# Kernel optimization log

Measured on AMD Instinct MI355X. Metric: run time of the kernel, lower is better.

Reference implementation:

```python
import jax, jax.numpy as jnp
import numpy as np

# Norse default LIFParameters
TAU_SYN_INV = 200.0  # 1/5e-3
TAU_MEM_INV = 100.0  # 1/1e-2
V_LEAK = 0.0
V_TH = 1.0
V_RESET = 0.0
DT = 0.001


def _heaviside(x):
    return (x > 0).astype(x.dtype)


def setup_inputs() -> dict:
    key = jax.random.key(0)
    k1, k2 = jax.random.split(key)
    T, B, F = 1024, 256, 512
    input_spikes = (jax.random.uniform(k1, (T, B, F)) < 0.1).astype(jnp.float32)
    W = jax.random.normal(k2, (F, F), dtype=jnp.float32) / np.sqrt(F).astype(np.float32)
    return {"input_spikes": input_spikes, "W": W}


def reference(input_spikes, W):
    # input_spikes: [T, B, F]; W: [F, F] (Linear, no bias)
    T, B, F = input_spikes.shape
    # fc batched across the whole sequence (y = x @ W.T)
    xs = jnp.einsum('tbf,gf->tbg', input_spikes, W)  # [T, B, F]
    v0 = jnp.zeros((B, F), dtype=input_spikes.dtype)
    i0 = jnp.zeros((B, F), dtype=input_spikes.dtype)

    def step(carry, x):
        v, i = carry
        v_dec = v + DT * TAU_MEM_INV * ((V_LEAK - v) + i)  # membrane leak+integrate
        i_dec = i - DT * TAU_SYN_INV * i                   # synaptic current decay
        z = _heaviside(v_dec - V_TH)                       # spike
        v_new = (1.0 - z) * v_dec + z * V_RESET            # reset
        i_new = i_dec + x                                  # inject fc output
        return (v_new, i_new), z

    (v, i), zs = jax.lax.scan(step, (v0, i0), xs)
    # matches torch forward: returns (z_last, state) with state = (v, i)
    return zs[-1], v, i
```

## Files before the change

### kernel.cpp

```cpp
#include <hip/hip_runtime.h>
#include <hip/hip_bf16.h>


typedef __attribute__((ext_vector_type(8))) short short8;
typedef __attribute__((ext_vector_type(4))) float floatx4;
typedef __attribute__((ext_vector_type(2))) unsigned uintx2;
typedef __attribute__((ext_vector_type(4))) unsigned uintx4;

#define T_STEPS 1024
#define B_DIM   256
#define F_DIM   512
#define BF      (B_DIM * F_DIM)
#define ROWP    520

static __device__ __forceinline__ unsigned short f2bf_rne(float f) {
    unsigned u = __float_as_uint(f);
    return (unsigned short)((u + 0x7FFFu + ((u >> 16) & 1u)) >> 16);
}
static __device__ __forceinline__ float bf2f(unsigned short h) {
    return __uint_as_float(((unsigned)h) << 16);
}

__global__ __launch_bounds__(256)
void pack_kernel(const float* __restrict__ sp, unsigned* __restrict__ bits)
{
    const int lane = threadIdx.x & 63;
    const int wv   = blockIdx.x * 4 + (threadIdx.x >> 6);
    for (int c = wv; c < 65536; c += 2048 * 4) {
        const float* p = sp + (size_t)c * 2048;
        unsigned val = 0;
        #pragma unroll
        for (int r = 0; r < 32; ++r) {
            float x = p[r * 64 + lane];
            unsigned long long m = __ballot(x != 0.0f);
            unsigned sel = (lane & 1) ? (unsigned)(m >> 32) : (unsigned)m;
            if ((lane >> 1) == r) val = sel;
        }
        bits[(size_t)c * 64 + lane] = val;
    }
}

__global__ __launch_bounds__(512, 4)
void lif_kernel_bits(const unsigned* __restrict__ bits,
                     const float* __restrict__ W,
                     float* __restrict__ out)
{
    __shared__ float xbuf[2][7 * 256];

    const int tid  = threadIdx.x;
    const int lane = tid & 63;
    const int wq   = tid >> 6;
    const int bt   = blockIdx.x & 15;
    const int gb   = blockIdx.x >> 4;
    const int b0   = bt * 16;
    const int gw   = gb * 16;
    const int mrow = lane & 15;
    const int lq   = lane >> 4;
    const int bsh  = lq * 8;

    short8 whi[2], wmd[2], wlo[2];
    {
        const float* wp = W + (size_t)(gw + mrow) * F_DIM + wq * 64 + lq * 8;
        #pragma unroll
        for (int ks = 0; ks < 2; ++ks) {
            short8 hi, md, lo;
            #pragma unroll
            for (int j = 0; j < 8; ++j) {
                float f = wp[ks * 32 + j];
                unsigned short h = f2bf_rne(f);
                float r1 = f - bf2f(h);
                unsigned short m = f2bf_rne(r1);
                float r2 = r1 - bf2f(m);
                hi[j] = (short)h;
                md[j] = (short)m;
                lo[j] = (short)f2bf_rne(r2);
            }
            whi[ks] = hi; wmd[ks] = md; wlo[ks] = lo;
        }
    }

    float v[4]  = {0.f, 0.f, 0.f, 0.f};
    float cu[4] = {0.f, 0.f, 0.f, 0.f};
    float zf[4] = {0.f, 0.f, 0.f, 0.f};

    const unsigned* bp = bits + (size_t)(b0 + mrow) * 16 + wq * 2;

    auto ldbits = [&](int t) -> uintx2 {
        return *(const uintx2*)(bp + (size_t)t * 4096);
    };

    auto expand = [&](uintx2 bq, short8* af) {
        #pragma unroll
        for (int ks = 0; ks < 2; ++ks) {
            unsigned b8 = (bq[ks] >> bsh) & 0xFFu;
            unsigned u  = b8 | (b8 << 15);
            unsigned x0 =  u        & 0x10001u;
            unsigned x1 = (u >> 2)  & 0x10001u;
            unsigned x2 = (u >> 4)  & 0x10001u;
            unsigned x3 = (u >> 6)  & 0x10001u;
            uintx4 d;
            d[0] = (x0 << 14) - (x0 << 7);
            d[1] = (x1 << 14) - (x1 << 7);
            d[2] = (x2 << 14) - (x2 << 7);
            d[3] = (x3 << 14) - (x3 << 7);
            af[ks] = *(short8*)&d;
        }
    };

    const floatx4 fz = {0.f, 0.f, 0.f, 0.f};

    auto mfma3 = [&](const short8* af, floatx4& ah, floatx4& am, floatx4& al) {
        ah = __builtin_amdgcn_mfma_f32_16x16x32_bf16(af[0], whi[0], fz, 0, 0, 0);
        am = __builtin_amdgcn_mfma_f32_16x16x32_bf16(af[0], wmd[0], fz, 0, 0, 0);
        al = __builtin_amdgcn_mfma_f32_16x16x32_bf16(af[0], wlo[0], fz, 0, 0, 0);
        ah = __builtin_amdgcn_mfma_f32_16x16x32_bf16(af[1], whi[1], ah, 0, 0, 0);
        am = __builtin_amdgcn_mfma_f32_16x16x32_bf16(af[1], wmd[1], am, 0, 0, 0);
        al = __builtin_amdgcn_mfma_f32_16x16x32_bf16(af[1], wlo[1], al, 0, 0, 0);
    };

    auto lif_step = [&](const floatx4& ah, const floatx4& am, const floatx4& al,
                        const float* xb) {
        floatx4 s;
        #pragma unroll
        for (int r = 0; r < 4; ++r) s[r] = (ah[r] + am[r]) + al[r];
        #pragma unroll
        for (int j = 0; j < 7; ++j) {
            floatx4 p = *(const floatx4*)(xb + j * 256 + lane * 4);
            #pragma unroll
            for (int r = 0; r < 4; ++r) s[r] += p[r];
        }
        #pragma unroll
        for (int r = 0; r < 4; ++r) {
            float x    = s[r];
            float vdec = v[r] + 0.1f * ((0.0f - v[r]) + cu[r]);
            float idec = cu[r] - 0.2f * cu[r];
            bool  spk  = (vdec - 1.0f) > 0.0f;
            zf[r] = spk ? 1.0f : 0.0f;
            v[r]  = spk ? 0.0f : vdec;
            cu[r] = idec + x;
        }
    };

    floatx4 ahA = fz, amA = fz, alA = fz;
    floatx4 ahB = fz, amB = fz, alB = fz;
    short8 afA[2], afB[2];

    uintx2 bqA = ldbits(0);
    uintx2 bqB = ldbits(1);

    for (int t = 0; t < T_STEPS; t += 2) {
        if (wq == 0 && t > 0)
            lif_step(ahB, amB, alB, &xbuf[1][0]);
        expand(bqA, afA);
        if (t + 2 < T_STEPS) bqA = ldbits(t + 2);
        mfma3(afA, ahA, amA, alA);
        if (wq > 0) {
            floatx4 xp;
            #pragma unroll
            for (int r = 0; r < 4; ++r) xp[r] = (ahA[r] + amA[r]) + alA[r];
            *(floatx4*)&xbuf[0][(wq - 1) * 256 + lane * 4] = xp;
        }
        __syncthreads();

        if (wq == 0)
            lif_step(ahA, amA, alA, &xbuf[0][0]);
        expand(bqB, afB);
        if (t + 3 < T_STEPS) bqB = ldbits(t + 3);
        mfma3(afB, ahB, amB, alB);
        if (wq > 0) {
            floatx4 xp;
            #pragma unroll
            for (int r = 0; r < 4; ++r) xp[r] = (ahB[r] + amB[r]) + alB[r];
            *(floatx4*)&xbuf[1][(wq - 1) * 256 + lane * 4] = xp;
        }
        __syncthreads();
    }
    if (wq == 0) {
        lif_step(ahB, amB, alB, &xbuf[1][0]);
        #pragma unroll
        for (int r = 0; r < 4; ++r) {
            const size_t idx = (size_t)(b0 + lq * 4 + r) * F_DIM + gw + mrow;
            out[idx]          = zf[r];
            out[BF + idx]     = v[r];
            out[2 * BF + idx] = cu[r];
        }
    }
}

__global__ __launch_bounds__(256, 1)
void lif_kernel_f32(const float* __restrict__ spikes,
                    const float* __restrict__ W,
                    float* __restrict__ out)
{
    __shared__ unsigned short sAf[16 * ROWP];
    __shared__ float xbuf[2 * 256];

    const int tid  = threadIdx.x;
    const int lane = tid & 63;
    const int w    = tid >> 6;
    const int gh   = w & 1;
    const int kh   = w >> 1;
    const int bt   = blockIdx.x & 15;
    const int gb   = blockIdx.x >> 4;
    const int b0   = bt * 16;
    const int gw   = gb * 32 + gh * 16;
    const int mrow = lane & 15;
    const int kq   = lane >> 4;

    short8 whi[8], wmd[8], wlo[8];
    {
        const float* wp = W + (size_t)(gw + mrow) * F_DIM + kh * 256 + kq * 8;
        #pragma unroll
        for (int ks = 0; ks < 8; ++ks) {
            short8 hi, md, lo;
            #pragma unroll
            for (int j = 0; j < 8; ++j) {
                float f = wp[ks * 32 + j];
                unsigned short h = f2bf_rne(f);
                float r1 = f - bf2f(h);
                unsigned short m = f2bf_rne(r1);
                float r2 = r1 - bf2f(m);
                hi[j] = (short)h;
                md[j] = (short)m;
                lo[j] = (short)f2bf_rne(r2);
            }
            whi[ks] = hi; wmd[ks] = md; wlo[ks] = lo;
        }
    }

    float v[4]  = {0.f, 0.f, 0.f, 0.f};
    float cu[4] = {0.f, 0.f, 0.f, 0.f};
    float zf[4] = {0.f, 0.f, 0.f, 0.f};

    floatx4 ld[8];
    auto issue_loads = [&](int t) {
        const floatx4* sp = (const floatx4*)(spikes + (size_t)t * BF + (size_t)b0 * F_DIM);
        #pragma unroll
        for (int j = 0; j < 8; ++j)
            ld[j] = sp[tid + 256 * j];
    };

    issue_loads(0);
    for (int t = 0; t < T_STEPS; ++t) {
        #pragma unroll
        for (int j = 0; j < 8; ++j) {
            const int q = tid + 256 * j;
            const int row = q >> 7, col4 = q & 127;
            unsigned u0 = __float_as_uint(ld[j][0]);
            unsigned u1 = __float_as_uint(ld[j][1]);
            unsigned u2 = __float_as_uint(ld[j][2]);
            unsigned u3 = __float_as_uint(ld[j][3]);
            uintx2 d;
            d[0] = (u0 >> 16) | (u1 & 0xFFFF0000u);
            d[1] = (u2 >> 16) | (u3 & 0xFFFF0000u);
            *(uintx2*)&sAf[row * ROWP + col4 * 4] = d;
        }
        __syncthreads();
        if (t + 1 < T_STEPS) issue_loads(t + 1);

        floatx4 ah = {0.f, 0.f, 0.f, 0.f};
        floatx4 am = {0.f, 0.f, 0.f, 0.f};
        floatx4 al = {0.f, 0.f, 0.f, 0.f};
        const unsigned short* arow = &sAf[mrow * ROWP + kh * 256 + kq * 8];
        #pragma unroll
        for (int ks = 0; ks < 8; ++ks) {
            short8 a = *(const short8*)(arow + ks * 32);
            ah = __builtin_amdgcn_mfma_f32_16x16x32_bf16(a, whi[ks], ah, 0, 0, 0);
            am = __builtin_amdgcn_mfma_f32_16x16x32_bf16(a, wmd[ks], am, 0, 0, 0);
            al = __builtin_amdgcn_mfma_f32_16x16x32_bf16(a, wlo[ks], al, 0, 0, 0);
        }

        if (kh == 1) {
            floatx4 xp = (ah + am) + al;
            *(floatx4*)&xbuf[gh * 256 + lane * 4] = xp;
        }
        __syncthreads();
        if (kh == 0) {
            floatx4 other = *(const floatx4*)&xbuf[gh * 256 + lane * 4];
            #pragma unroll
            for (int r = 0; r < 4; ++r) {
                float x    = ((ah[r] + am[r]) + al[r]) + other[r];
                float vdec = v[r] + 0.1f * ((0.0f - v[r]) + cu[r]);
                float idec = cu[r] - 0.2f * cu[r];
                bool  spk  = (vdec - 1.0f) > 0.0f;
                zf[r] = spk ? 1.0f : 0.0f;
                v[r]  = spk ? 0.0f : vdec;
                cu[r] = idec + x;
            }
        }
    }

    if (kh == 0) {
        #pragma unroll
        for (int r = 0; r < 4; ++r) {
            const size_t idx = (size_t)(b0 + kq * 4 + r) * F_DIM + gw + mrow;
            out[idx]          = zf[r];
            out[BF + idx]     = v[r];
            out[2 * BF + idx] = cu[r];
        }
    }
}

extern "C" void kernel_launch(void* const* d_in, const int* in_sizes, int n_in,
                              void* d_out, int out_size, void* d_ws, size_t ws_size,
                              hipStream_t stream)
{
    const float* spikes = (const float*)d_in[0];
    const float* W      = (const float*)d_in[1];
    float* out          = (float*)d_out;

    const size_t need = (size_t)T_STEPS * B_DIM * (F_DIM / 8);
    if (d_ws != nullptr && ws_size >= need) {
        unsigned* bits = (unsigned*)d_ws;
        pack_kernel<<<dim3(2048), dim3(256), 0, stream>>>(spikes, bits);
        lif_kernel_bits<<<dim3(512), dim3(512), 0, stream>>>(bits, W, out);
    } else {
        lif_kernel_f32<<<dim3(256), dim3(256), 0, stream>>>(spikes, W, out);
    }
}
```

Measured before the change: 1.223 ms.

## Replace bf16 triple-split MFMA with int8 three-digit fixed-point MFMA

The weights are quantized per output row to a 24-bit fixed-point integer, scaled by the row max, and split into three signed int8 digits. Binary spikes are expanded straight into int8 operands. One i32_16x16x64_i8 MFMA per digit replaces the six bf16 MFMAs, and the partial sums are recombined in float and rescaled in the LIF step. This cuts MFMA count and spike-expansion work per timestep. The cost is a fixed-point approximation with about 2^-23 relative error against the row max, plus an extra shared-memory reduction and barrier at setup.

```diff
diff --git a/kernel.cpp b/kernel.cpp
--- a/kernel.cpp
+++ b/kernel.cpp
@@ -5,7 +5,7 @@
 typedef __attribute__((ext_vector_type(8))) short short8;
 typedef __attribute__((ext_vector_type(4))) float floatx4;
 typedef __attribute__((ext_vector_type(2))) unsigned uintx2;
-typedef __attribute__((ext_vector_type(4))) unsigned uintx4;
+typedef __attribute__((ext_vector_type(4))) int int4v;
 
 #define T_STEPS 1024
 #define B_DIM   256
@@ -46,6 +46,7 @@
                      float* __restrict__ out)
 {
     __shared__ float xbuf[2][7 * 256];
+    __shared__ float rowmax[8][16];
 
     const int tid  = threadIdx.x;
     const int lane = tid & 63;
@@ -56,26 +57,43 @@
     const int gw   = gb * 16;
     const int mrow = lane & 15;
     const int lq   = lane >> 4;
-    const int bsh  = lq * 8;
-
-    short8 whi[2], wmd[2], wlo[2];
+
+    int4v wi0, wi1, wi2;
+    float invC;
     {
-        const float* wp = W + (size_t)(gw + mrow) * F_DIM + wq * 64 + lq * 8;
-        #pragma unroll
-        for (int ks = 0; ks < 2; ++ks) {
-            short8 hi, md, lo;
+        const float* wp = W + (size_t)(gw + mrow) * F_DIM + wq * 64 + lq * 16;
+        float wv[16];
+        float lm = 0.0f;
+        #pragma unroll
+        for (int j = 0; j < 16; ++j) {
+            wv[j] = wp[j];
+            lm = fmaxf(lm, fabsf(wv[j]));
+        }
+        lm = fmaxf(lm, __shfl_xor(lm, 16, 64));
+        lm = fmaxf(lm, __shfl_xor(lm, 32, 64));
+        if (lane < 16) rowmax[wq][lane] = lm;
+        __syncthreads();
+        float S = 1e-30f;
+        #pragma unroll
+        for (int w8 = 0; w8 < 8; ++w8) S = fmaxf(S, rowmax[w8][mrow]);
+        __syncthreads();
+        const float C = 8000000.0f / S;
+        invC = S / 8000000.0f;
+        #pragma unroll
+        for (int d = 0; d < 4; ++d) {
+            unsigned p0 = 0, p1 = 0, p2 = 0;
             #pragma unroll
-            for (int j = 0; j < 8; ++j) {
-                float f = wp[ks * 32 + j];
-                unsigned short h = f2bf_rne(f);
-                float r1 = f - bf2f(h);
-                unsigned short m = f2bf_rne(r1);
-                float r2 = r1 - bf2f(m);
-                hi[j] = (short)h;
-                md[j] = (short)m;
-                lo[j] = (short)f2bf_rne(r2);
+            for (int jj = 0; jj < 4; ++jj) {
+                int q  = __float2int_rn(wv[d * 4 + jj] * C);
+                int d2 = (q << 24) >> 24;
+                int r1 = (q - d2) >> 8;
+                int d1 = (r1 << 24) >> 24;
+                int d0 = (r1 - d1) >> 8;
+                p0 |= (unsigned)(d0 & 0xFF) << (8 * jj);
+                p1 |= (unsigned)(d1 & 0xFF) << (8 * jj);
+                p2 |= (unsigned)(d2 & 0xFF) << (8 * jj);
             }
-            whi[ks] = hi; wmd[ks] = md; wlo[ks] = lo;
+            wi0[d] = (int)p0; wi1[d] = (int)p1; wi2[d] = (int)p2;
         }
     }
 
@@ -89,40 +107,37 @@
         return *(const uintx2*)(bp + (size_t)t * 4096);
     };
 
-    auto expand = [&](uintx2 bq, short8* af) {
-        #pragma unroll
-        for (int ks = 0; ks < 2; ++ks) {
-            unsigned b8 = (bq[ks] >> bsh) & 0xFFu;
-            unsigned u  = b8 | (b8 << 15);
-            unsigned x0 =  u        & 0x10001u;
-            unsigned x1 = (u >> 2)  & 0x10001u;
-            unsigned x2 = (u >> 4)  & 0x10001u;
-            unsigned x3 = (u >> 6)  & 0x10001u;
-            uintx4 d;
-            d[0] = (x0 << 14) - (x0 << 7);
-            d[1] = (x1 << 14) - (x1 << 7);
-            d[2] = (x2 << 14) - (x2 << 7);
-            d[3] = (x3 << 14) - (x3 << 7);
-            af[ks] = *(short8*)&d;
-        }
-    };
-
-    const floatx4 fz = {0.f, 0.f, 0.f, 0.f};
-
-    auto mfma3 = [&](const short8* af, floatx4& ah, floatx4& am, floatx4& al) {
-        ah = __builtin_amdgcn_mfma_f32_16x16x32_bf16(af[0], whi[0], fz, 0, 0, 0);
-        am = __builtin_amdgcn_mfma_f32_16x16x32_bf16(af[0], wmd[0], fz, 0, 0, 0);
-        al = __builtin_amdgcn_mfma_f32_16x16x32_bf16(af[0], wlo[0], fz, 0, 0, 0);
-        ah = __builtin_amdgcn_mfma_f32_16x16x32_bf16(af[1], whi[1], ah, 0, 0, 0);
-        am = __builtin_amdgcn_mfma_f32_16x16x32_bf16(af[1], wmd[1], am, 0, 0, 0);
-        al = __builtin_amdgcn_mfma_f32_16x16x32_bf16(af[1], wlo[1], al, 0, 0, 0);
-    };
-
-    auto lif_step = [&](const floatx4& ah, const floatx4& am, const floatx4& al,
-                        const float* xb) {
-        floatx4 s;
-        #pragma unroll
-        for (int r = 0; r < 4; ++r) s[r] = (ah[r] + am[r]) + al[r];
+    auto expand = [&](uintx2 bq) -> int4v {
+        unsigned h16 = ((lq & 2) ? bq[1] : bq[0]) >> ((lq & 1) * 16);
+        int4v a;
+        #pragma unroll
+        for (int d = 0; d < 4; ++d) {
+            unsigned b4 = (h16 >> (4 * d)) & 0xFu;
+            unsigned u  = (b4 << 7) + b4;
+            u = (b4 << 14) + u;
+            u = (b4 << 21) + u;
+            a[d] = (int)(u & 0x01010101u);
+        }
+        return a;
+    };
+
+    const int4v iz = {0, 0, 0, 0};
+
+    auto mfma_combine = [&](int4v aI) -> floatx4 {
+        int4v acc0 = __builtin_amdgcn_mfma_i32_16x16x64_i8(aI, wi0, iz, 0, 0, 0);
+        int4v acc1 = __builtin_amdgcn_mfma_i32_16x16x64_i8(aI, wi1, iz, 0, 0, 0);
+        int4v acc2 = __builtin_amdgcn_mfma_i32_16x16x64_i8(aI, wi2, iz, 0, 0, 0);
+        floatx4 M;
+        #pragma unroll
+        for (int r = 0; r < 4; ++r) {
+            int a12 = (acc1[r] << 8) + acc2[r];
+            M[r] = fmaf((float)acc0[r], 65536.0f, (float)a12);
+        }
+        return M;
+    };
+
+    auto lif_step = [&](const floatx4& Mown, const float* xb) {
+        floatx4 s = Mown;
         #pragma unroll
         for (int j = 0; j < 7; ++j) {
             floatx4 p = *(const floatx4*)(xb + j * 256 + lane * 4);
@@ -131,7 +146,7 @@
         }
         #pragma unroll
         for (int r = 0; r < 4; ++r) {
-            float x    = s[r];
+            float x    = s[r] * invC;
             float vdec = v[r] + 0.1f * ((0.0f - v[r]) + cu[r]);
             float idec = cu[r] - 0.2f * cu[r];
             bool  spk  = (vdec - 1.0f) > 0.0f;
@@ -141,42 +156,37 @@
         }
     };
 
-    floatx4 ahA = fz, amA = fz, alA = fz;
-    floatx4 ahB = fz, amB = fz, alB = fz;
-    short8 afA[2], afB[2];
+    floatx4 MA = {0.f, 0.f, 0.f, 0.f};
+    floatx4 MB = {0.f, 0.f, 0.f, 0.f};
 
     uintx2 bqA = ldbits(0);
     uintx2 bqB = ldbits(1);
 
     for (int t = 0; t < T_STEPS; t += 2) {
         if (wq == 0 && t > 0)
-            lif_step(ahB, amB, alB, &xbuf[1][0]);
-        expand(bqA, afA);
-        if (t + 2 < T_STEPS) bqA = ldbits(t + 2);
-        mfma3(afA, ahA, amA, alA);
-        if (wq > 0) {
-            floatx4 xp;
-            #pragma unroll
-            for (int r = 0; r < 4; ++r) xp[r] = (ahA[r] + amA[r]) + alA[r];
-            *(floatx4*)&xbuf[0][(wq - 1) * 256 + lane * 4] = xp;
+            lif_step(MB, &xbuf[1][0]);
+        {
+            int4v aI = expand(bqA);
+            if (t + 2 < T_STEPS) bqA = ldbits(t + 2);
+            floatx4 M = mfma_combine(aI);
+            if (wq > 0) *(floatx4*)&xbuf[0][(wq - 1) * 256 + lane * 4] = M;
+            else        MA = M;
         }
         __syncthreads();
 
         if (wq == 0)
-            lif_step(ahA, amA, alA, &xbuf[0][0]);
-        expand(bqB, afB);
-        if (t + 3 < T_STEPS) bqB = ldbits(t + 3);
-        mfma3(afB, ahB, amB, alB);
-        if (wq > 0) {
-            floatx4 xp;
-            #pragma unroll
-            for (int r = 0; r < 4; ++r) xp[r] = (ahB[r] + amB[r]) + alB[r];
-            *(floatx4*)&xbuf[1][(wq - 1) * 256 + lane * 4] = xp;
+            lif_step(MA, &xbuf[0][0]);
+        {
+            int4v aI = expand(bqB);
+            if (t + 3 < T_STEPS) bqB = ldbits(t + 3);
+            floatx4 M = mfma_combine(aI);
+            if (wq > 0) *(floatx4*)&xbuf[1][(wq - 1) * 256 + lane * 4] = M;
+            else        MB = M;
         }
         __syncthreads();
     }
     if (wq == 0) {
-        lif_step(ahB, amB, alB, &xbuf[1][0]);
+        lif_step(MB, &xbuf[1][0]);
         #pragma unroll
         for (int r = 0; r < 4; ++r) {
             const size_t idx = (size_t)(b0 + lq * 4 + r) * F_DIM + gw + mrow;
```

Result: faster. 1.147 ms (-6.2%).
